# Optimization experiments

Hardware: AMD Instinct MI355X
Metric: run time of the kernel (lower is better)

## Reference

```python
import jax, jax.numpy as jnp
import numpy as np

D = 1024
H = 16
HD = D // H


def quant_linear(x, W, b):
    # global abs-max fake quant, then linear (W is [out, in] like torch)
    scale = jnp.abs(x).max() / 127.0 + 1e-8
    xq = jnp.clip(jnp.round(x / scale), -128.0, 127.0) * scale
    return xq @ W.T + b


def rmsnorm(x, w, eps=1e-6):
    ms = jnp.mean(x * x, axis=-1, keepdims=True)
    return w * (x * jax.lax.rsqrt(ms + eps))


def setup_inputs() -> dict:
    key = jax.random.key(0)
    ks = jax.random.split(key, 20)
    def lin(k, out_f, in_f):
        bound = 1.0 / np.sqrt(in_f)
        kw, kb = jax.random.split(k)
        W = jax.random.uniform(kw, (out_f, in_f), jnp.float32, -bound, bound)
        b = jax.random.uniform(kb, (out_f,), jnp.float32, -bound, bound)
        return W, b
    x = jax.random.normal(ks[0], (4, 2048, D), jnp.float32)
    h_prev = jax.random.normal(ks[1], (4, 2048, D), jnp.float32)
    rec_W, rec_b = lin(ks[2], D, D)
    in_proj_w = jax.random.normal(ks[3], (3 * D, D), jnp.float32) * (1.0 / np.sqrt(D))
    in_proj_b = jnp.zeros((3 * D,), jnp.float32)
    out_w, out_b = lin(ks[4], D, D)
    w1_W, w1_b = lin(ks[5], 4 * D, D)
    w2_W, w2_b = lin(ks[6], 4 * D, D)
    w3_W, w3_b = lin(ks[7], D, 4 * D)
    # depthwise conv1d: torch weight [D, 1, 5]
    cb = 1.0 / np.sqrt(5)
    conv_w = jax.random.uniform(ks[8], (D, 1, 5), jnp.float32, -cb, cb)
    conv_b = jax.random.uniform(ks[9], (D,), jnp.float32, -cb, cb)
    return dict(x=x, h_prev=h_prev,
                norm1_w=jnp.ones((D,), jnp.float32), norm2_w=jnp.ones((D,), jnp.float32),
                decay=jnp.full((D,), -0.2, jnp.float32),
                rec_W=rec_W, rec_b=rec_b,
                in_proj_w=in_proj_w, in_proj_b=in_proj_b, out_w=out_w, out_b=out_b,
                conv_w=conv_w, conv_b=conv_b,
                w1_W=w1_W, w1_b=w1_b, w2_W=w2_W, w2_b=w2_b, w3_W=w3_W, w3_b=w3_b)


def reference(x, h_prev, norm1_w, norm2_w, decay, rec_W, rec_b,
              in_proj_w, in_proj_b, out_w, out_b, conv_w, conv_b,
              w1_W, w1_b, w2_W, w2_b, w3_W, w3_b):
    B, S, _ = x.shape
    nx = rmsnorm(x, norm1_w)
    # decay-gated recurrence (single step)
    h_rec = jnp.tanh(quant_linear(nx, rec_W, rec_b) + jnp.exp(decay) * h_prev)
    # multi-head self-attention (torch MultiheadAttention, batch_first)
    qkv = nx @ in_proj_w.T + in_proj_b  # [B,S,3D]
    q, k, v = jnp.split(qkv, 3, axis=-1)
    q = q.reshape(B, S, H, HD)
    k = k.reshape(B, S, H, HD)
    v = v.reshape(B, S, H, HD)
    scores = jnp.einsum('bqhd,bkhd->bhqk', q, k) / np.sqrt(HD)
    attn = jax.nn.softmax(scores, axis=-1)
    h_attn = jnp.einsum('bhqk,bkhd->bqhd', attn, v).reshape(B, S, D)
    h_attn = h_attn @ out_w.T + out_b
    # depthwise conv along sequence
    xc = jnp.swapaxes(nx, 1, 2)  # [B,D,S]
    hc = jax.lax.conv_general_dilated(xc, conv_w, window_strides=(1,), padding=[(2, 2)],
                                      feature_group_count=D,
                                      dimension_numbers=('NCH', 'OIH', 'NCH'))
    h_conv = jnp.swapaxes(hc + conv_b[None, :, None], 1, 2)
    x = x + h_rec + h_attn + h_conv
    # SwiGLU FFN with fake-quant linears
    nx2 = rmsnorm(x, norm2_w)
    ff = quant_linear(jax.nn.silu(quant_linear(nx2, w1_W, w1_b)) * quant_linear(nx2, w2_W, w2_b), w3_W, w3_b)
    x = x + ff
    return (x, h_rec)
```

## Files before the change

### kernel.cpp

```cpp
#include <hip/hip_runtime.h>
#include <stdint.h>

#define DD 1024
#define SS 2048
#define HH 16
#define HDD 64
#define NTOK 8192

typedef unsigned short u16;
typedef __attribute__((ext_vector_type(8))) short bf16x8;
typedef __attribute__((ext_vector_type(4))) float f32x4;
typedef __attribute__((ext_vector_type(4))) u16 u16x4;
typedef __attribute__((address_space(1))) unsigned int u32a1;
typedef __attribute__((address_space(3))) unsigned int u32a3;

__device__ __forceinline__ float bf2f(u16 u){
  union { float f; unsigned v; } c; c.v = ((unsigned)u) << 16; return c.f;
}
__device__ __forceinline__ u16 f2bf(float f){
  unsigned x = __float_as_uint(f);
  x = (x + 0x7fffu + ((x >> 16) & 1u)) >> 16;
  return (u16)x;
}
__device__ __forceinline__ void async16(const u16* g, u16* l){
  __builtin_amdgcn_global_load_lds((const u32a1*)g, (u32a3*)l, 16, 0, 0);
}


__global__ __launch_bounds__(256) void f32_to_bf16_kernel(
    const float* __restrict__ in, u16* __restrict__ out, int n)
{
  int i = (blockIdx.x * 256 + threadIdx.x) * 4;
  if (i >= n) return;
  float4 v = *(const float4*)(in + i);
  u16x4 o; o.x = f2bf(v.x); o.y = f2bf(v.y); o.z = f2bf(v.z); o.w = f2bf(v.w);
  *(u16x4*)(out + i) = o;
}

__global__ __launch_bounds__(256) void rmsnorm_absmax_kernel(
    const float* __restrict__ xin, const float* __restrict__ wgt,
    u16* __restrict__ nxo, float* __restrict__ pmax)
{
  const int row = blockIdx.x, t = threadIdx.x;
  const int w = t >> 6, l = t & 63;
  float4 xv = *(const float4*)(xin + (size_t)row * DD + t * 4);
  float ss = xv.x*xv.x + xv.y*xv.y + xv.z*xv.z + xv.w*xv.w;
  #pragma unroll
  for (int m = 1; m < 64; m <<= 1) ss += __shfl_xor(ss, m, 64);
  __shared__ float red[4];
  __shared__ float redm[4];
  if (l == 0) red[w] = ss;
  __syncthreads();
  float tot = red[0] + red[1] + red[2] + red[3];
  float rstd = rsqrtf(tot * (1.f / DD) + 1e-6f);
  float4 wv = *(const float4*)(wgt + t * 4);
  float o0 = xv.x * rstd * wv.x;
  float o1 = xv.y * rstd * wv.y;
  float o2 = xv.z * rstd * wv.z;
  float o3 = xv.w * rstd * wv.w;
  u16x4 ov; ov.x = f2bf(o0); ov.y = f2bf(o1); ov.z = f2bf(o2); ov.w = f2bf(o3);
  *(u16x4*)(nxo + (size_t)row * DD + t * 4) = ov;
  float lm = fmaxf(fmaxf(fabsf(o0), fabsf(o1)), fmaxf(fabsf(o2), fabsf(o3)));
  #pragma unroll
  for (int m = 1; m < 64; m <<= 1) lm = fmaxf(lm, __shfl_xor(lm, m, 64));
  if (l == 0) redm[w] = lm;
  __syncthreads();
  if (t == 0)
    pmax[row] = fmaxf(fmaxf(redm[0], redm[1]), fmaxf(redm[2], redm[3]));
}

__global__ __launch_bounds__(1024) void amax_reduce_kernel(
    const float* __restrict__ p, int n, unsigned* __restrict__ amax)
{
  const int t = threadIdx.x;
  float m = 0.f;
  for (int i = t; i < n; i += 1024) m = fmaxf(m, p[i]);
  #pragma unroll
  for (int msk = 1; msk < 64; msk <<= 1) m = fmaxf(m, __shfl_xor(m, msk, 64));
  __shared__ float red[16];
  if ((t & 63) == 0) red[t >> 6] = m;
  __syncthreads();
  if (t == 0){
    float mm = red[0];
    #pragma unroll
    for (int i = 1; i < 16; i++) mm = fmaxf(mm, red[i]);
    *amax = __float_as_uint(mm);
  }
}

__global__ __launch_bounds__(256) void quantize_kernel(
    const u16* __restrict__ in, u16* __restrict__ outq,
    const unsigned* __restrict__ amax, int n)
{
  int i = (blockIdx.x * 256 + threadIdx.x) * 8;
  if (i >= n) return;
  float am = __uint_as_float(*amax);
  float scale = am / 127.f + 1e-8f;
  float inv = 1.f / scale;
  uint4 a = *(const uint4*)(in + i);
  u16* u = (u16*)&a;
  #pragma unroll
  for (int j = 0; j < 8; j++){
    float v = bf2f(u[j]);
    float q = rintf(v * inv);
    q = fminf(127.f, fmaxf(-128.f, q));
    u[j] = f2bf(q * scale);
  }
  *(uint4*)(outq + i) = a;
}

template<int MODE>
__global__ __launch_bounds__(256) void gemm_bt(
    const u16* __restrict__ A, const u16* __restrict__ Wt,
    const float* __restrict__ bias, int M, int N, int K,
    void* __restrict__ out,
    const float* __restrict__ e0, const float* __restrict__ e1,
    const float* __restrict__ e2, const float* __restrict__ e3,
    const u16* __restrict__ eb0, float* __restrict__ pmax)
{
  __shared__ __align__(16) u16 Ash[128 * 32];
  __shared__ __align__(16) u16 Bsh[128 * 32];
  const int t = threadIdx.x, w = t >> 6, l = t & 63;
  const int brow = blockIdx.y * 128, bcol = blockIdx.x * 128;
  const int wr = w >> 1, wc = w & 1;
  f32x4 acc[4][4] = {};

  const u16* Ab = A + (size_t)brow * K;
  const u16* Bb = Wt + (size_t)bcol * K;
  const int r4 = t >> 2, c8 = (t & 3) * 8;

  for (int k0 = 0; k0 < K; k0 += 32){
    #pragma unroll
    for (int j = 0; j < 2; j++){
      async16(Ab + (size_t)(j * 64 + r4) * K + k0 + c8, &Ash[(j * 64 + r4) * 32 + c8]);
      async16(Bb + (size_t)(j * 64 + r4) * K + k0 + c8, &Bsh[(j * 64 + r4) * 32 + c8]);
    }
    __syncthreads();
    bf16x8 af[4], bfr[4];
    #pragma unroll
    for (int m = 0; m < 4; m++)
      af[m] = *(const bf16x8*)&Ash[(wr * 64 + m * 16 + (l & 15)) * 32 + (l >> 4) * 8];
    #pragma unroll
    for (int n = 0; n < 4; n++)
      bfr[n] = *(const bf16x8*)&Bsh[(wc * 64 + n * 16 + (l & 15)) * 32 + (l >> 4) * 8];
    #pragma unroll
    for (int m = 0; m < 4; m++)
      #pragma unroll
      for (int n = 0; n < 4; n++)
        acc[m][n] = __builtin_amdgcn_mfma_f32_16x16x32_bf16(af[m], bfr[n], acc[m][n], 0, 0, 0);
    __syncthreads();
  }

  float localmax = 0.f;
  #pragma unroll
  for (int m = 0; m < 4; m++){
    #pragma unroll
    for (int n = 0; n < 4; n++){
      #pragma unroll
      for (int r = 0; r < 4; r++){
        const int row = brow + wr * 64 + m * 16 + (l >> 4) * 4 + r;
        const int col = bcol + wc * 64 + n * 16 + (l & 15);
        const size_t idx = (size_t)row * N + col;
        float v = acc[m][n][r] + bias[col];
        if constexpr (MODE == 0){
          ((u16*)out)[idx] = f2bf(v);
        } else if constexpr (MODE == 1){
          v = tanhf(v + expf(e0[col]) * e1[idx]);
          ((float*)out)[idx] = v;
        } else if constexpr (MODE == 2){
          const int s = row & (SS - 1);
          float hc = e3[col];
          const u16* np = eb0 + idx;
          #pragma unroll
          for (int j = 0; j < 5; j++){
            int sn = s + j - 2;
            if (sn >= 0 && sn < SS) hc += bf2f(np[(j - 2) * DD]) * e2[col * 5 + j];
          }
          ((float*)out)[idx] = v + e0[idx] + e1[idx] + hc;
        } else if constexpr (MODE == 3){
          float h1v = bf2f(eb0[idx]);
          float g = h1v / (1.f + expf(-h1v)) * v;
          ((u16*)out)[idx] = f2bf(g);
          localmax = fmaxf(localmax, fabsf(g));
        } else {
          ((float*)out)[idx] += v;
        }
      }
    }
  }
  if constexpr (MODE == 3){
    #pragma unroll
    for (int msk = 1; msk < 64; msk <<= 1)
      localmax = fmaxf(localmax, __shfl_xor(localmax, msk, 64));
    __shared__ float wmax[4];
    if (l == 0) wmax[w] = localmax;
    __syncthreads();
    if (t == 0)
      pmax[blockIdx.y * gridDim.x + blockIdx.x] =
          fmaxf(fmaxf(wmax[0], wmax[1]), fmaxf(wmax[2], wmax[3]));
  }
}

__global__ __launch_bounds__(256) void attn_kernel(
    const u16* __restrict__ qkv, u16* __restrict__ attn_out)
{
  const int qb = blockIdx.x;
  const int bh = blockIdx.y;
  const int h = bh & (HH - 1), b = bh >> 4;
  const int t = threadIdx.x, w = t >> 6, l = t & 63;
  const int tok0 = b * SS;
  const size_t rstr = 3 * DD;

  __shared__ __align__(16) u16 Ksh[64 * 64];
  __shared__ __align__(16) u16 Vsh[64 * 80];
  __shared__ __align__(16) u16 Psh[4][16 * 80];

  const int qr0 = qb * 64 + w * 16;
  bf16x8 qf[2];
  {
    const u16* qp = qkv + (size_t)(tok0 + qr0 + (l & 15)) * rstr + h * HDD + (l >> 4) * 8;
    qf[0] = *(const bf16x8*)qp;
    qf[1] = *(const bf16x8*)(qp + 32);
  }
  f32x4 acc_o[4] = {};
  float mrun[4], lrun[4];
  #pragma unroll
  for (int r = 0; r < 4; r++){ mrun[r] = -1e30f; lrun[r] = 0.f; }

  for (int kv0 = 0; kv0 < SS; kv0 += 64){
    #pragma unroll
    for (int j = 0; j < 2; j++){
      const int krl = j * 32 + (t >> 3);
      const int c8 = (t & 7) * 8;
      const size_t rowb = (size_t)(tok0 + kv0 + krl) * rstr;
      uint4 kv4 = *(const uint4*)(qkv + rowb + DD + h * HDD + c8);
      int bo = (krl * 64 + c8) * 2; bo ^= (krl & 7) << 4;
      *(uint4*)((char*)Ksh + bo) = kv4;
      uint4 vv4 = *(const uint4*)(qkv + rowb + 2 * DD + h * HDD + c8);
      const u16* vs = (const u16*)&vv4;
      #pragma unroll
      for (int i = 0; i < 8; i++) Vsh[(c8 + i) * 80 + krl] = vs[i];
    }
    __syncthreads();

    f32x4 sc[4];
    #pragma unroll
    for (int n = 0; n < 4; n++){
      f32x4 z = {};
      #pragma unroll
      for (int kk = 0; kk < 2; kk++){
        const int krow = n * 16 + (l & 15);
        int bo = (krow * 64 + kk * 32 + (l >> 4) * 8) * 2; bo ^= (krow & 7) << 4;
        bf16x8 kf = *(const bf16x8*)((const char*)Ksh + bo);
        z = __builtin_amdgcn_mfma_f32_16x16x32_bf16(qf[kk], kf, z, 0, 0, 0);
      }
      sc[n] = z * 0.125f;
    }

    #pragma unroll
    for (int r = 0; r < 4; r++){
      float m0 = fmaxf(fmaxf(sc[0][r], sc[1][r]), fmaxf(sc[2][r], sc[3][r]));
      #pragma unroll
      for (int msk = 1; msk < 16; msk <<= 1) m0 = fmaxf(m0, __shfl_xor(m0, msk, 64));
      float mn = fmaxf(mrun[r], m0);
      float al = __expf(mrun[r] - mn);
      mrun[r] = mn;
      lrun[r] *= al;
      #pragma unroll
      for (int n = 0; n < 4; n++) acc_o[n][r] *= al;
    }
    float rsum[4] = {0.f, 0.f, 0.f, 0.f};
    #pragma unroll
    for (int n = 0; n < 4; n++)
      #pragma unroll
      for (int r = 0; r < 4; r++){
        float p = __expf(sc[n][r] - mrun[r]);
        sc[n][r] = p;
        rsum[r] += p;
      }
    #pragma unroll
    for (int r = 0; r < 4; r++){
      #pragma unroll
      for (int msk = 1; msk < 16; msk <<= 1) rsum[r] += __shfl_xor(rsum[r], msk, 64);
      lrun[r] += rsum[r];
    }

    #pragma unroll
    for (int n = 0; n < 4; n++)
      #pragma unroll
      for (int r = 0; r < 4; r++)
        Psh[w][((l >> 4) * 4 + r) * 80 + n * 16 + (l & 15)] = f2bf(sc[n][r]);
    __syncthreads();

    #pragma unroll
    for (int kk = 0; kk < 2; kk++){
      bf16x8 pf = *(const bf16x8*)&Psh[w][(l & 15) * 80 + kk * 32 + (l >> 4) * 8];
      #pragma unroll
      for (int n = 0; n < 4; n++){
        bf16x8 vf = *(const bf16x8*)&Vsh[(n * 16 + (l & 15)) * 80 + kk * 32 + (l >> 4) * 8];
        acc_o[n] = __builtin_amdgcn_mfma_f32_16x16x32_bf16(pf, vf, acc_o[n], 0, 0, 0);
      }
    }
    __syncthreads();
  }

  #pragma unroll
  for (int r = 0; r < 4; r++){
    float inv = 1.f / lrun[r];
    const int row = tok0 + qr0 + (l >> 4) * 4 + r;
    #pragma unroll
    for (int n = 0; n < 4; n++)
      attn_out[(size_t)row * DD + h * HDD + n * 16 + (l & 15)] = f2bf(acc_o[n][r] * inv);
  }
}


extern "C" void kernel_launch(void* const* d_in, const int* in_sizes, int n_in,
                              void* d_out, int out_size, void* d_ws, size_t ws_size,
                              hipStream_t stream)
{
  (void)in_sizes; (void)n_in; (void)out_size; (void)ws_size;
  const float* x       = (const float*)d_in[0];
  const float* h_prev  = (const float*)d_in[1];
  const float* norm1_w = (const float*)d_in[2];
  const float* norm2_w = (const float*)d_in[3];
  const float* decay   = (const float*)d_in[4];
  const float* rec_W   = (const float*)d_in[5];
  const float* rec_b   = (const float*)d_in[6];
  const float* inp_W   = (const float*)d_in[7];
  const float* inp_b   = (const float*)d_in[8];
  const float* out_W   = (const float*)d_in[9];
  const float* out_b   = (const float*)d_in[10];
  const float* conv_w  = (const float*)d_in[11];
  const float* conv_b  = (const float*)d_in[12];
  const float* w1_W    = (const float*)d_in[13];
  const float* w1_b    = (const float*)d_in[14];
  const float* w2_W    = (const float*)d_in[15];
  const float* w2_b    = (const float*)d_in[16];
  const float* w3_W    = (const float*)d_in[17];
  const float* w3_b    = (const float*)d_in[18];

  const size_t NDe = (size_t)NTOK * DD;
  float* out_x = (float*)d_out;
  float* out_h = (float*)d_out + NDe;

  char* ws = (char*)d_ws;
  unsigned* amax1 = (unsigned*)ws;
  unsigned* amax2 = amax1 + 1;
  unsigned* amax3 = amax1 + 2;
  size_t off = 256;
  u16* Wrec = (u16*)(ws + off); off += (size_t)DD * DD * 2;
  u16* Winp = (u16*)(ws + off); off += (size_t)3 * DD * DD * 2;
  u16* Wout = (u16*)(ws + off); off += (size_t)DD * DD * 2;
  u16* W1   = (u16*)(ws + off); off += (size_t)4 * DD * DD * 2;
  u16* W2   = (u16*)(ws + off); off += (size_t)4 * DD * DD * 2;
  u16* W3   = (u16*)(ws + off); off += (size_t)4 * DD * DD * 2;
  u16* nx   = (u16*)(ws + off); off += NDe * 2;
  u16* xq   = (u16*)(ws + off); off += NDe * 2;
  u16* big  = (u16*)(ws + off); off += (size_t)NTOK * 4096 * 2;
  float* pmax1 = (float*)(ws + off); off += NTOK * 4;
  float* pmax2 = (float*)(ws + off); off += NTOK * 4;
  float* pmax3 = (float*)(ws + off); off += 2048 * 4;
  u16* qkvp    = big;
  u16* attnout = big + (size_t)NTOK * 3 * DD;

  f32_to_bf16_kernel<<<dim3(1024),  dim3(256), 0, stream>>>(rec_W, Wrec, DD * DD);
  f32_to_bf16_kernel<<<dim3(3072),  dim3(256), 0, stream>>>(inp_W, Winp, 3 * DD * DD);
  f32_to_bf16_kernel<<<dim3(1024),  dim3(256), 0, stream>>>(out_W, Wout, DD * DD);
  f32_to_bf16_kernel<<<dim3(4096),  dim3(256), 0, stream>>>(w1_W, W1, 4 * DD * DD);
  f32_to_bf16_kernel<<<dim3(4096),  dim3(256), 0, stream>>>(w2_W, W2, 4 * DD * DD);
  f32_to_bf16_kernel<<<dim3(4096),  dim3(256), 0, stream>>>(w3_W, W3, 4 * DD * DD);

  rmsnorm_absmax_kernel<<<dim3(NTOK), dim3(256), 0, stream>>>(x, norm1_w, nx, pmax1);
  amax_reduce_kernel<<<dim3(1), dim3(1024), 0, stream>>>(pmax1, NTOK, amax1);
  quantize_kernel<<<dim3(4096), dim3(256), 0, stream>>>(nx, xq, amax1, (int)NDe);

  gemm_bt<1><<<dim3(8, 64), dim3(256), 0, stream>>>(xq, Wrec, rec_b, NTOK, DD, DD,
      out_h, decay, h_prev, nullptr, nullptr, nullptr, nullptr);
  gemm_bt<0><<<dim3(24, 64), dim3(256), 0, stream>>>(nx, Winp, inp_b, NTOK, 3 * DD, DD,
      qkvp, nullptr, nullptr, nullptr, nullptr, nullptr, nullptr);
  attn_kernel<<<dim3(32, 64), dim3(256), 0, stream>>>(qkvp, attnout);
  gemm_bt<2><<<dim3(8, 64), dim3(256), 0, stream>>>(attnout, Wout, out_b, NTOK, DD, DD,
      out_x, x, out_h, conv_w, conv_b, nx, nullptr);

  rmsnorm_absmax_kernel<<<dim3(NTOK), dim3(256), 0, stream>>>(out_x, norm2_w, nx, pmax2);
  amax_reduce_kernel<<<dim3(1), dim3(1024), 0, stream>>>(pmax2, NTOK, amax2);
  quantize_kernel<<<dim3(4096), dim3(256), 0, stream>>>(nx, xq, amax2, (int)NDe);
  gemm_bt<0><<<dim3(32, 64), dim3(256), 0, stream>>>(xq, W1, w1_b, NTOK, 4 * DD, DD,
      big, nullptr, nullptr, nullptr, nullptr, nullptr, nullptr);
  gemm_bt<3><<<dim3(32, 64), dim3(256), 0, stream>>>(xq, W2, w2_b, NTOK, 4 * DD, DD,
      big, nullptr, nullptr, nullptr, nullptr, big, pmax3);
  amax_reduce_kernel<<<dim3(1), dim3(1024), 0, stream>>>(pmax3, 2048, amax3);
  quantize_kernel<<<dim3(16384), dim3(256), 0, stream>>>(big, big, amax3, NTOK * 4096);
  gemm_bt<4><<<dim3(8, 64), dim3(256), 0, stream>>>(big, W3, w3_b, NTOK, DD, 4 * DD,
      out_x, nullptr, nullptr, nullptr, nullptr, nullptr, nullptr);
}
```

Measured before the change: 1.125 ms.

## Process two query tiles per wave in attention to reuse K/V tiles

Each wave in the attention kernel now handles 32 query rows as two 16-row tiles, so every block covers 128 queries and the grid is halved. Each K/V tile staged in shared memory is reused across twice as many queries, which cuts global K/V traffic and the V-transpose store work per query. The padded V and P shared-memory layouts become XOR-swizzled 64-wide layouts, and the block-wide barrier between the P write and the PV MFMA is dropped because P is private to each wave. In exchange, register pressure rises from the doubled accumulators and softmax state, and the smaller grid may lower occupancy or balance across CUs.

```diff
diff --git a/kernel.cpp b/kernel.cpp
--- a/kernel.cpp
+++ b/kernel.cpp
@@ -24,6 +24,9 @@
 }
 __device__ __forceinline__ void async16(const u16* g, u16* l){
   __builtin_amdgcn_global_load_lds((const u32a1*)g, (u32a3*)l, 16, 0, 0);
+}
+__device__ __forceinline__ int vswz(int row){
+  return (((row & 7) ^ ((row >> 3) & 7)) << 4);
 }
 
 
@@ -208,110 +211,130 @@
   const int bh = blockIdx.y;
   const int h = bh & (HH - 1), b = bh >> 4;
   const int t = threadIdx.x, w = t >> 6, l = t & 63;
+  const int lm = l & 15, lh = l >> 4;
   const int tok0 = b * SS;
   const size_t rstr = 3 * DD;
 
   __shared__ __align__(16) u16 Ksh[64 * 64];
-  __shared__ __align__(16) u16 Vsh[64 * 80];
-  __shared__ __align__(16) u16 Psh[4][16 * 80];
-
-  const int qr0 = qb * 64 + w * 16;
-  bf16x8 qf[2];
-  {
-    const u16* qp = qkv + (size_t)(tok0 + qr0 + (l & 15)) * rstr + h * HDD + (l >> 4) * 8;
-    qf[0] = *(const bf16x8*)qp;
-    qf[1] = *(const bf16x8*)(qp + 32);
-  }
-  f32x4 acc_o[4] = {};
-  float mrun[4], lrun[4];
-  #pragma unroll
-  for (int r = 0; r < 4; r++){ mrun[r] = -1e30f; lrun[r] = 0.f; }
+  __shared__ __align__(16) u16 Vsh[64 * 64];
+  __shared__ __align__(16) u16 Psh[4][32 * 64];
+
+  const int qr0 = qb * 128 + w * 32;
+  bf16x8 qf[2][2];
+  #pragma unroll
+  for (int qt = 0; qt < 2; qt++){
+    const u16* qp = qkv + (size_t)(tok0 + qr0 + qt * 16 + lm) * rstr + h * HDD + lh * 8;
+    qf[qt][0] = *(const bf16x8*)qp;
+    qf[qt][1] = *(const bf16x8*)(qp + 32);
+  }
+  f32x4 acc_o[2][4] = {};
+  float mrun[2][4], lrun[2][4];
+  #pragma unroll
+  for (int qt = 0; qt < 2; qt++)
+    #pragma unroll
+    for (int r = 0; r < 4; r++){ mrun[qt][r] = -1e30f; lrun[qt][r] = 0.f; }
 
   for (int kv0 = 0; kv0 < SS; kv0 += 64){
     #pragma unroll
     for (int j = 0; j < 2; j++){
       const int krl = j * 32 + (t >> 3);
       const int c8 = (t & 7) * 8;
-      const size_t rowb = (size_t)(tok0 + kv0 + krl) * rstr;
-      uint4 kv4 = *(const uint4*)(qkv + rowb + DD + h * HDD + c8);
-      int bo = (krl * 64 + c8) * 2; bo ^= (krl & 7) << 4;
-      *(uint4*)((char*)Ksh + bo) = kv4;
-      uint4 vv4 = *(const uint4*)(qkv + rowb + 2 * DD + h * HDD + c8);
+      const size_t rowb = (size_t)(tok0 + kv0 + krl) * rstr + h * HDD + c8;
+      uint4 kv4 = *(const uint4*)(qkv + rowb + DD);
+      *(uint4*)((char*)Ksh + (((krl * 64 + c8) * 2) ^ ((krl & 7) << 4))) = kv4;
+      uint4 vv4 = *(const uint4*)(qkv + rowb + 2 * DD);
       const u16* vs = (const u16*)&vv4;
       #pragma unroll
-      for (int i = 0; i < 8; i++) Vsh[(c8 + i) * 80 + krl] = vs[i];
+      for (int i = 0; i < 8; i++){
+        const int vr = c8 + i;
+        *(u16*)((char*)Vsh + (((vr * 64 + krl) * 2) ^ vswz(vr))) = vs[i];
+      }
     }
     __syncthreads();
 
-    f32x4 sc[4];
-    #pragma unroll
-    for (int n = 0; n < 4; n++){
-      f32x4 z = {};
-      #pragma unroll
-      for (int kk = 0; kk < 2; kk++){
-        const int krow = n * 16 + (l & 15);
-        int bo = (krow * 64 + kk * 32 + (l >> 4) * 8) * 2; bo ^= (krow & 7) << 4;
-        bf16x8 kf = *(const bf16x8*)((const char*)Ksh + bo);
-        z = __builtin_amdgcn_mfma_f32_16x16x32_bf16(qf[kk], kf, z, 0, 0, 0);
-      }
-      sc[n] = z * 0.125f;
-    }
-
+    #pragma unroll
+    for (int qt = 0; qt < 2; qt++){
+      f32x4 sc[4];
+      #pragma unroll
+      for (int n = 0; n < 4; n++){
+        f32x4 z = {};
+        #pragma unroll
+        for (int kk = 0; kk < 2; kk++){
+          const int krow = n * 16 + lm;
+          bf16x8 kf = *(const bf16x8*)((const char*)Ksh +
+              (((krow * 64 + kk * 32 + lh * 8) * 2) ^ ((krow & 7) << 4)));
+          z = __builtin_amdgcn_mfma_f32_16x16x32_bf16(qf[qt][kk], kf, z, 0, 0, 0);
+        }
+        sc[n] = z * 0.125f;
+      }
+      #pragma unroll
+      for (int r = 0; r < 4; r++){
+        float m0 = fmaxf(fmaxf(sc[0][r], sc[1][r]), fmaxf(sc[2][r], sc[3][r]));
+        #pragma unroll
+        for (int msk = 1; msk < 16; msk <<= 1) m0 = fmaxf(m0, __shfl_xor(m0, msk, 64));
+        float mn = fmaxf(mrun[qt][r], m0);
+        float al = __expf(mrun[qt][r] - mn);
+        mrun[qt][r] = mn;
+        lrun[qt][r] *= al;
+        #pragma unroll
+        for (int n = 0; n < 4; n++) acc_o[qt][n][r] *= al;
+      }
+      float rsum[4] = {0.f, 0.f, 0.f, 0.f};
+      #pragma unroll
+      for (int n = 0; n < 4; n++)
+        #pragma unroll
+        for (int r = 0; r < 4; r++){
+          float p = __expf(sc[n][r] - mrun[qt][r]);
+          sc[n][r] = p;
+          rsum[r] += p;
+        }
+      #pragma unroll
+      for (int r = 0; r < 4; r++){
+        #pragma unroll
+        for (int msk = 1; msk < 16; msk <<= 1) rsum[r] += __shfl_xor(rsum[r], msk, 64);
+        lrun[qt][r] += rsum[r];
+      }
+      #pragma unroll
+      for (int n = 0; n < 4; n++)
+        #pragma unroll
+        for (int r = 0; r < 4; r++){
+          const int prow = qt * 16 + lh * 4 + r;
+          *(u16*)((char*)&Psh[w][0] +
+              (((prow * 64 + n * 16 + lm) * 2) ^ vswz(prow))) = f2bf(sc[n][r]);
+        }
+    }
+
+    #pragma unroll
+    for (int kk = 0; kk < 2; kk++){
+      bf16x8 pf[2];
+      #pragma unroll
+      for (int qt = 0; qt < 2; qt++){
+        const int prow = qt * 16 + lm;
+        pf[qt] = *(const bf16x8*)((const char*)&Psh[w][0] +
+            (((prow * 64 + kk * 32 + lh * 8) * 2) ^ vswz(prow)));
+      }
+      #pragma unroll
+      for (int n = 0; n < 4; n++){
+        const int vr = n * 16 + lm;
+        bf16x8 vf = *(const bf16x8*)((const char*)Vsh +
+            (((vr * 64 + kk * 32 + lh * 8) * 2) ^ vswz(vr)));
+        acc_o[0][n] = __builtin_amdgcn_mfma_f32_16x16x32_bf16(pf[0], vf, acc_o[0][n], 0, 0, 0);
+        acc_o[1][n] = __builtin_amdgcn_mfma_f32_16x16x32_bf16(pf[1], vf, acc_o[1][n], 0, 0, 0);
+      }
+    }
+    __syncthreads();
+  }
+
+  #pragma unroll
+  for (int qt = 0; qt < 2; qt++)
     #pragma unroll
     for (int r = 0; r < 4; r++){
-      float m0 = fmaxf(fmaxf(sc[0][r], sc[1][r]), fmaxf(sc[2][r], sc[3][r]));
-      #pragma unroll
-      for (int msk = 1; msk < 16; msk <<= 1) m0 = fmaxf(m0, __shfl_xor(m0, msk, 64));
-      float mn = fmaxf(mrun[r], m0);
-      float al = __expf(mrun[r] - mn);
-      mrun[r] = mn;
-      lrun[r] *= al;
-      #pragma unroll
-      for (int n = 0; n < 4; n++) acc_o[n][r] *= al;
-    }
-    float rsum[4] = {0.f, 0.f, 0.f, 0.f};
-    #pragma unroll
-    for (int n = 0; n < 4; n++)
-      #pragma unroll
-      for (int r = 0; r < 4; r++){
-        float p = __expf(sc[n][r] - mrun[r]);
-        sc[n][r] = p;
-        rsum[r] += p;
-      }
-    #pragma unroll
-    for (int r = 0; r < 4; r++){
-      #pragma unroll
-      for (int msk = 1; msk < 16; msk <<= 1) rsum[r] += __shfl_xor(rsum[r], msk, 64);
-      lrun[r] += rsum[r];
-    }
-
-    #pragma unroll
-    for (int n = 0; n < 4; n++)
-      #pragma unroll
-      for (int r = 0; r < 4; r++)
-        Psh[w][((l >> 4) * 4 + r) * 80 + n * 16 + (l & 15)] = f2bf(sc[n][r]);
-    __syncthreads();
-
-    #pragma unroll
-    for (int kk = 0; kk < 2; kk++){
-      bf16x8 pf = *(const bf16x8*)&Psh[w][(l & 15) * 80 + kk * 32 + (l >> 4) * 8];
-      #pragma unroll
-      for (int n = 0; n < 4; n++){
-        bf16x8 vf = *(const bf16x8*)&Vsh[(n * 16 + (l & 15)) * 80 + kk * 32 + (l >> 4) * 8];
-        acc_o[n] = __builtin_amdgcn_mfma_f32_16x16x32_bf16(pf, vf, acc_o[n], 0, 0, 0);
-      }
-    }
-    __syncthreads();
-  }
-
-  #pragma unroll
-  for (int r = 0; r < 4; r++){
-    float inv = 1.f / lrun[r];
-    const int row = tok0 + qr0 + (l >> 4) * 4 + r;
-    #pragma unroll
-    for (int n = 0; n < 4; n++)
-      attn_out[(size_t)row * DD + h * HDD + n * 16 + (l & 15)] = f2bf(acc_o[n][r] * inv);
-  }
+      float inv = 1.f / lrun[qt][r];
+      const int row = tok0 + qr0 + qt * 16 + lh * 4 + r;
+      #pragma unroll
+      for (int n = 0; n < 4; n++)
+        attn_out[(size_t)row * DD + h * HDD + n * 16 + lm] = f2bf(acc_o[qt][n][r] * inv);
+    }
 }
 
 
@@ -379,7 +402,7 @@
       out_h, decay, h_prev, nullptr, nullptr, nullptr, nullptr);
   gemm_bt<0><<<dim3(24, 64), dim3(256), 0, stream>>>(nx, Winp, inp_b, NTOK, 3 * DD, DD,
       qkvp, nullptr, nullptr, nullptr, nullptr, nullptr, nullptr);
-  attn_kernel<<<dim3(32, 64), dim3(256), 0, stream>>>(qkvp, attnout);
+  attn_kernel<<<dim3(16, 64), dim3(256), 0, stream>>>(qkvp, attnout);
   gemm_bt<2><<<dim3(8, 64), dim3(256), 0, stream>>>(attnout, Wout, out_b, NTOK, DD, DD,
       out_x, x, out_h, conv_w, conv_b, nx, nullptr);
 
```

Result: faster. 1.076 ms (-4.3%).
